# Kernel optimization log

Hardware: AMD Instinct MI355X
Metric: run time of the kernel (lower is better)

Reference implementation:

```python
import jax, jax.numpy as jnp
import numpy as np

N = 177          # hardcoded in update(): view(1, 177, out_channels)
HEADS = 1
OUT = 128
EDGE_DIM = 1
NEG_SLOPE = 0.2
E = 500000


def _glorot(key, shape):
    stdv = np.sqrt(6.0 / (shape[-2] + shape[-1])).astype(np.float32)
    return jax.random.uniform(key, shape, jnp.float32, -stdv, stdv)


def setup_inputs() -> dict:
    key = jax.random.key(0)
    ks = jax.random.split(key, 6)
    x = jax.random.normal(ks[0], (1, N, 128), jnp.float32)
    edge_index = jax.random.randint(ks[1], (2, E), 0, N)
    edge_attr = jax.random.normal(ks[2], (E, EDGE_DIM), jnp.float32)
    weight = _glorot(ks[3], (128, HEADS * OUT))
    att = _glorot(ks[4], (1, HEADS, 2 * OUT + EDGE_DIM))
    edge_update1 = _glorot(ks[5], (OUT + EDGE_DIM, OUT))
    bias = jnp.zeros((OUT,), jnp.float32)
    return {"x": x, "edge_attr": edge_attr, "weight": weight, "att": att,
            "edge_update1": edge_update1, "bias": bias, "edge_index": edge_index}


def reference(x, edge_attr, weight, att, edge_update1, bias, edge_index):
    # node transform: [N, in] @ [in, H*C] -> [N, H, C]
    h = (x[0] @ weight).reshape(-1, HEADS, OUT)
    src, dst = edge_index[0], edge_index[1]   # PyG: row 0 = source (j), row 1 = target (i)
    x_j = h[src]                              # [E, H, C]
    x_i = h[dst]                              # [E, H, C]
    ea = jnp.broadcast_to(edge_attr[:, None, :], (edge_attr.shape[0], HEADS, EDGE_DIM))
    x_j = jnp.concatenate([x_j, ea], axis=-1)              # [E, H, C+edge_dim]
    # attention logits: sum over feature axis of cat([x_i, x_j]) * att
    alpha = (jnp.concatenate([x_i, x_j], axis=-1) * att).sum(axis=-1)  # [E, H]
    alpha = jax.nn.leaky_relu(alpha, NEG_SLOPE)
    # scatter softmax over target nodes (two-pass: segment max then segment sum)
    amax = jax.ops.segment_max(alpha, dst, num_segments=N)             # [N, H]
    e = jnp.exp(alpha - amax[dst])
    esum = jax.ops.segment_sum(e, dst, num_segments=N)                 # [N, H]
    alpha = e / (esum[dst] + 1e-16)
    # weighted messages, scatter-add aggregation
    msg = x_j * alpha[:, :, None]                                      # [E, H, C+edge_dim]
    aggr = jax.ops.segment_sum(msg, dst, num_segments=N)               # [N, H, C+edge_dim]
    out = aggr.mean(axis=1) @ edge_update1 + bias                      # [N, C]
    return out.reshape(1, N, OUT)
```

## Files before the change

### kernel.cpp

```cpp
#include <hip/hip_runtime.h>

#define NN 177
#define NEG 0.2f
#define QR 45
#define ROWP 180
#define QSLOTS_P (QR * ROWP)
#define SL 8192
#define NCHUNK 64
#define EBLOCKS (NCHUNK * 4)
#define ETH 512

#define AIP_OFF  0
#define AJP_OFF  384
#define PART_OFF 768

__device__ __forceinline__ float4 f4add(float4 a, float4 b) {
    return make_float4(a.x + b.x, a.y + b.y, a.z + b.z, a.w + b.w);
}

__global__ __launch_bounds__(256)
void k_nodeA(const float* __restrict__ x, const float* __restrict__ w,
             const float* __restrict__ att, float* __restrict__ ws) {
    const int n = blockIdx.x, half = blockIdx.y;
    const int tid = threadIdx.x;
    const int j = tid & 63, kq = tid >> 6;
    __shared__ float xl[128];
    __shared__ float ph[256];
    if (tid < 128) xl[tid] = x[n * 128 + tid];
    __syncthreads();
    const float* wp = w + (size_t)(kq * 32) * 128 + half * 64 + j;
    float acc = 0.f;
#pragma unroll 8
    for (int k = 0; k < 32; ++k) acc += xl[kq * 32 + k] * wp[(size_t)k * 128];
    ph[tid] = acc;
    __syncthreads();
    if (tid < 64) {
        float hv = ph[j] + ph[64 + j] + ph[128 + j] + ph[192 + j];
        float pa = hv * att[half * 64 + j];
        float pb = hv * att[128 + half * 64 + j];
#pragma unroll
        for (int m = 1; m < 64; m <<= 1) {
            pa += __shfl_xor(pa, m);
            pb += __shfl_xor(pb, m);
        }
        if (j == 0) {
            ws[AIP_OFF + 2 * n + half] = pa;
            ws[AJP_OFF + 2 * n + half] = pb;
        }
    }
}

__global__ __launch_bounds__(ETH, 8)
void k_edge(const int* __restrict__ ei, const float* __restrict__ ea,
            const float* __restrict__ att, float* __restrict__ ws, int E, int CH) {
    const int chunk = blockIdx.x & (NCHUNK - 1), q = blockIdx.x >> 6;
    const int dlo = q * QR;
    int drows = NN - dlo; if (drows > QR) drows = QR;
    __shared__ __align__(16) float Wl[QSLOTS_P];
    __shared__ float ajl[NN], ailq[QR], Mq[QR], llast[QR], mred[64];
    int tid = threadIdx.x;
    const float4 z4 = make_float4(0.f, 0.f, 0.f, 0.f);
    for (int i = tid; i < QSLOTS_P / 4; i += ETH) ((float4*)Wl)[i] = z4;
    for (int i = tid; i < NN; i += ETH)
        ajl[i] = ws[AJP_OFF + 2 * i] + ws[AJP_OFF + 2 * i + 1];
    if (tid < QR) llast[tid] = 0.f;
    __syncthreads();
    if (tid < 64) {
        float m = -1e30f;
        for (int i = tid; i < NN; i += 64) m = fmaxf(m, ajl[i]);
        mred[tid] = m;
    }
    __syncthreads();
    if (tid < 16) mred[tid] = fmaxf(fmaxf(mred[tid], mred[tid + 16]),
                                    fmaxf(mred[tid + 32], mred[tid + 48]));
    __syncthreads();
    if (tid < 4) mred[tid] = fmaxf(fmaxf(mred[tid], mred[tid + 4]),
                                   fmaxf(mred[tid + 8], mred[tid + 12]));
    __syncthreads();
    if (tid == 0) mred[0] = fmaxf(fmaxf(mred[0], mred[1]), fmaxf(mred[2], mred[3]));
    __syncthreads();
    const float ajmax = mred[0];
    if (tid < drows) {
        float a = ws[AIP_OFF + 2 * (dlo + tid)] + ws[AIP_OFF + 2 * (dlo + tid) + 1];
        ailq[tid] = a;
        float M = a + ajmax + 1.0f;
        Mq[tid] = (M > 0.f) ? M : NEG * M;
    }
    const float cc = att[2 * 128];
    __syncthreads();

    const int base = chunk * CH;
    int lim = base + CH; if (lim > E) lim = E;
    const bool aligned4 = ((E & 3) == 0);
    for (int e0 = base + tid * 4; e0 < lim; e0 += ETH * 4) {
        int4 sv, dv; float4 eav;
        if (aligned4 && e0 + 3 < lim) {
            sv  = *(const int4*)(ei + e0);
            dv  = *(const int4*)(ei + E + e0);
            eav = *(const float4*)(ea + e0);
        } else {
            int e1 = lim - e0;
            sv.x = (e1 > 0) ? ei[e0]     : 0; dv.x = (e1 > 0) ? ei[E + e0]     : -1; eav.x = (e1 > 0) ? ea[e0]     : 0.f;
            sv.y = (e1 > 1) ? ei[e0 + 1] : 0; dv.y = (e1 > 1) ? ei[E + e0 + 1] : -1; eav.y = (e1 > 1) ? ea[e0 + 1] : 0.f;
            sv.z = (e1 > 2) ? ei[e0 + 2] : 0; dv.z = (e1 > 2) ? ei[E + e0 + 2] : -1; eav.z = (e1 > 2) ? ea[e0 + 2] : 0.f;
            sv.w = (e1 > 3) ? ei[e0 + 3] : 0; dv.w = (e1 > 3) ? ei[E + e0 + 3] : -1; eav.w = (e1 > 3) ? ea[e0 + 3] : 0.f;
        }
#define PROC(SS, DD, EE) do {                                   \
            int d_ = (DD) - dlo;                                \
            if ((unsigned)d_ < (unsigned)drows) {               \
                float t_ = ailq[d_] + ajl[SS] + cc * (EE);      \
                t_ = (t_ > 0.f) ? t_ : NEG * t_;                \
                float ev_ = __expf(t_ - Mq[d_]);                \
                atomicAdd(&Wl[d_ * ROWP + (SS)], ev_);          \
                atomicAdd(&llast[d_], ev_ * (EE));              \
            }                                                   \
        } while (0)
        PROC(sv.x, dv.x, eav.x);
        PROC(sv.y, dv.y, eav.y);
        PROC(sv.z, dv.z, eav.z);
        PROC(sv.w, dv.w, eav.w);
#undef PROC
    }
    __syncthreads();
    float* part = ws + PART_OFF + (size_t)blockIdx.x * SL;
    for (int i = tid; i < QSLOTS_P / 4; i += ETH)
        ((float4*)part)[i] = ((const float4*)Wl)[i];
    if (tid < QR) part[QSLOTS_P + tid] = llast[tid];
}

__global__ __launch_bounds__(ETH)
void k_outD(const float* __restrict__ ws, const float* __restrict__ x,
            const float* __restrict__ w, const float* __restrict__ eu,
            const float* __restrict__ bias, float* __restrict__ out) {
    __shared__ __align__(16) float wl[ROWP];
    __shared__ float red[128];
    __shared__ float sc[2];
    __shared__ float yl[128], vl[128];
    __shared__ __align__(16) float pd[2048];
    const int n = blockIdx.x, tid = threadIdx.x;
    const int q = n / QR, r = n % QR;
    const size_t qbase = PART_OFF + (size_t)q * NCHUNK * SL;

    {
        const int lane = tid & 63, cg = tid >> 6;
        const int s4 = lane * 4;
        float4 acc = make_float4(0.f, 0.f, 0.f, 0.f);
        if (s4 < ROWP) {
            const float* p = ws + qbase + (size_t)(cg * 8) * SL + (size_t)r * ROWP + s4;
#pragma unroll
            for (int ch = 0; ch < 8; ++ch)
                acc = f4add(acc, *(const float4*)(p + (size_t)ch * SL));
        }
        ((float4*)pd)[tid] = acc;
    }
    if (tid < 64) red[tid] = ws[qbase + (size_t)tid * SL + QSLOTS_P + r];
    __syncthreads();
    if (tid < 256) ((float4*)pd)[tid] = f4add(((float4*)pd)[tid], ((float4*)pd)[tid + 256]);
    if (tid < 32) red[tid] += red[tid + 32];
    __syncthreads();
    if (tid < 128) ((float4*)pd)[tid] = f4add(((float4*)pd)[tid], ((float4*)pd)[tid + 128]);
    if (tid < 16) red[tid] += red[tid + 16];
    __syncthreads();
    if (tid < 64) {
        float4 v = f4add(((float4*)pd)[tid], ((float4*)pd)[tid + 64]);
        if (tid * 4 < ROWP) ((float4*)wl)[tid] = v;
    }
    if (tid < 8) red[tid] += red[tid + 8];
    __syncthreads();
    if (tid == 0) {
        float wv = 0.f;
#pragma unroll
        for (int i = 0; i < 8; ++i) wv += red[i];
        sc[0] = wv;
    }
    __syncthreads();
    if (tid < 128) red[tid] = wl[tid] + ((tid + 128 < NN) ? wl[tid + 128] : 0.f);
    __syncthreads();
    for (int off = 64; off > 0; off >>= 1) {
        if (tid < off) red[tid] += red[tid + off];
        __syncthreads();
    }
    if (tid == 0) sc[1] = red[0];
    __syncthreads();

    const int c = tid & 127, g = tid >> 7;

    {
        float acc = 0.f;
        int s0 = g * 45, s1 = s0 + 45; if (s1 > NN) s1 = NN;
        for (int s = s0; s < s1; ++s) acc += wl[s] * x[s * 128 + c];
        pd[tid] = acc;
    }
    __syncthreads();
    if (tid < 128) yl[tid] = (pd[tid] + pd[128 + tid]) + (pd[256 + tid] + pd[384 + tid]);
    __syncthreads();

    {
        float acc = 0.f;
        const float* wp = w + (size_t)(g * 32) * 128 + c;
#pragma unroll 8
        for (int k = 0; k < 32; ++k) acc += yl[g * 32 + k] * wp[(size_t)k * 128];
        pd[tid] = acc;
    }
    __syncthreads();
    if (tid < 128) vl[tid] = (pd[tid] + pd[128 + tid]) + (pd[256 + tid] + pd[384 + tid]);
    __syncthreads();

    {
        float acc = 0.f;
        const float* ep = eu + (size_t)(g * 32) * 128 + c;
#pragma unroll 8
        for (int k = 0; k < 32; ++k) acc += vl[g * 32 + k] * ep[(size_t)k * 128];
        pd[tid] = acc;
    }
    __syncthreads();
    if (tid < 128) {
        float dot = (pd[tid] + pd[128 + tid]) + (pd[256 + tid] + pd[384 + tid]);
        out[n * 128 + tid] = (dot + sc[0] * eu[128 * 128 + tid]) / (sc[1] + 1e-16f) + bias[tid];
    }
}

extern "C" void kernel_launch(void* const* d_in, const int* in_sizes, int n_in,
                              void* d_out, int out_size, void* d_ws, size_t ws_size,
                              hipStream_t stream) {
    const float* x     = (const float*)d_in[0];
    const float* eattr = (const float*)d_in[1];
    const float* w     = (const float*)d_in[2];
    const float* att   = (const float*)d_in[3];
    const float* eu    = (const float*)d_in[4];
    const float* bias  = (const float*)d_in[5];
    const int*   ei    = (const int*)d_in[6];
    int E = in_sizes[6] / 2;
    int CH = (((E + NCHUNK - 1) / NCHUNK) + 3) & ~3;
    float* ws = (float*)d_ws;

    k_nodeA<<<dim3(NN, 2), 256, 0, stream>>>(x, w, att, ws);
    k_edge<<<EBLOCKS, ETH, 0, stream>>>(ei, eattr, att, ws, E, CH);
    k_outD<<<NN, ETH, 0, stream>>>(ws, x, w, eu, bias, (float*)d_out);
}
```

Before: 32.24 us.

## Fuse node attention projection into edge kernel via precomputed W·att vectors

Measured after the change: 34.71 us. 1.08x slower.

```diff
diff --git a/kernel.cpp b/kernel.cpp
--- a/kernel.cpp
+++ b/kernel.cpp
@@ -9,62 +9,76 @@
 #define NCHUNK 64
 #define EBLOCKS (NCHUNK * 4)
 #define ETH 512
-
-#define AIP_OFF  0
-#define AJP_OFF  384
+#define XFLOATS (NN * 128)
+
 #define PART_OFF 768
 
 __device__ __forceinline__ float4 f4add(float4 a, float4 b) {
     return make_float4(a.x + b.x, a.y + b.y, a.z + b.z, a.w + b.w);
 }
 
-__global__ __launch_bounds__(256)
-void k_nodeA(const float* __restrict__ x, const float* __restrict__ w,
-             const float* __restrict__ att, float* __restrict__ ws) {
-    const int n = blockIdx.x, half = blockIdx.y;
+__global__ __launch_bounds__(ETH)
+void k_edgeA(const float* __restrict__ x, const float* __restrict__ ea,
+             const float* __restrict__ w, const float* __restrict__ att,
+             const int* __restrict__ ei, float* __restrict__ ws, int E, int CH) {
+    extern __shared__ __align__(16) float big[];
+    __shared__ float atl[257], uvec[128], vvec[128];
+    __shared__ float pa_arr[2 * NN], pb_arr[2 * NN];
+    __shared__ float ail[NN], ajl[NN], Mq[QR], llast[QR], mred[64];
     const int tid = threadIdx.x;
-    const int j = tid & 63, kq = tid >> 6;
-    __shared__ float xl[128];
-    __shared__ float ph[256];
-    if (tid < 128) xl[tid] = x[n * 128 + tid];
-    __syncthreads();
-    const float* wp = w + (size_t)(kq * 32) * 128 + half * 64 + j;
-    float acc = 0.f;
-#pragma unroll 8
-    for (int k = 0; k < 32; ++k) acc += xl[kq * 32 + k] * wp[(size_t)k * 128];
-    ph[tid] = acc;
-    __syncthreads();
-    if (tid < 64) {
-        float hv = ph[j] + ph[64 + j] + ph[128 + j] + ph[192 + j];
-        float pa = hv * att[half * 64 + j];
-        float pb = hv * att[128 + half * 64 + j];
-#pragma unroll
-        for (int m = 1; m < 64; m <<= 1) {
-            pa += __shfl_xor(pa, m);
-            pb += __shfl_xor(pb, m);
-        }
-        if (j == 0) {
-            ws[AIP_OFF + 2 * n + half] = pa;
-            ws[AJP_OFF + 2 * n + half] = pb;
-        }
-    }
-}
-
-__global__ __launch_bounds__(ETH, 8)
-void k_edge(const int* __restrict__ ei, const float* __restrict__ ea,
-            const float* __restrict__ att, float* __restrict__ ws, int E, int CH) {
-    const int chunk = blockIdx.x & (NCHUNK - 1), q = blockIdx.x >> 6;
+    const int bid = blockIdx.x;
+    const int chunk = bid & (NCHUNK - 1), q = bid >> 6;
     const int dlo = q * QR;
     int drows = NN - dlo; if (drows > QR) drows = QR;
-    __shared__ __align__(16) float Wl[QSLOTS_P];
-    __shared__ float ajl[NN], ailq[QR], Mq[QR], llast[QR], mred[64];
-    int tid = threadIdx.x;
-    const float4 z4 = make_float4(0.f, 0.f, 0.f, 0.f);
-    for (int i = tid; i < QSLOTS_P / 4; i += ETH) ((float4*)Wl)[i] = z4;
-    for (int i = tid; i < NN; i += ETH)
-        ajl[i] = ws[AJP_OFF + 2 * i] + ws[AJP_OFF + 2 * i + 1];
-    if (tid < QR) llast[tid] = 0.f;
-    __syncthreads();
+
+    for (int i = tid; i < 257; i += ETH) atl[i] = att[i];
+    __syncthreads();
+
+    const float4* w4 = (const float4*)w;
+#pragma unroll
+    for (int i = 0; i < 8; ++i) {
+        int f = i * 512 + tid;
+        int k = f >> 5, c4 = (f & 31) << 2;
+        float4 wv = w4[f];
+        float pu = wv.x*atl[c4]     + wv.y*atl[c4+1]     + wv.z*atl[c4+2]     + wv.w*atl[c4+3];
+        float pv = wv.x*atl[128+c4] + wv.y*atl[128+c4+1] + wv.z*atl[128+c4+2] + wv.w*atl[128+c4+3];
+#pragma unroll
+        for (int m = 1; m <= 16; m <<= 1) { pu += __shfl_xor(pu, m); pv += __shfl_xor(pv, m); }
+        if ((tid & 31) == 0) { uvec[k] = pu; vvec[k] = pv; }
+    }
+
+    {
+        const float4* x4 = (const float4*)x;
+        float4* b4 = (float4*)big;
+        for (int i = tid; i < XFLOATS / 4; i += ETH) b4[i] = x4[i];
+    }
+    __syncthreads();
+
+    {
+        const int r = (tid < NN) ? tid : tid - NN;
+        const int h = (tid < NN) ? 0 : 1;
+        if (tid < 2 * NN) {
+            const float* xr = big + r * 128 + h * 64;
+            const float* ur = uvec + h * 64;
+            const float* vr = vvec + h * 64;
+            float pa = 0.f, pb = 0.f;
+#pragma unroll 8
+            for (int kk = 0; kk < 64; ++kk) {
+                int k = (kk + r) & 63;
+                float xv = xr[k];
+                pa += xv * ur[k];
+                pb += xv * vr[k];
+            }
+            pa_arr[tid] = pa; pb_arr[tid] = pb;
+        }
+    }
+    __syncthreads();
+    if (tid < NN) {
+        ail[tid] = pa_arr[tid] + pa_arr[NN + tid];
+        ajl[tid] = pb_arr[tid] + pb_arr[NN + tid];
+    }
+    __syncthreads();
+
     if (tid < 64) {
         float m = -1e30f;
         for (int i = tid; i < NN; i += 64) m = fmaxf(m, ajl[i]);
@@ -80,13 +94,16 @@
     if (tid == 0) mred[0] = fmaxf(fmaxf(mred[0], mred[1]), fmaxf(mred[2], mred[3]));
     __syncthreads();
     const float ajmax = mred[0];
+
+    float* Wl = big;
+    const float4 z4 = make_float4(0.f, 0.f, 0.f, 0.f);
+    for (int i = tid; i < QSLOTS_P / 4; i += ETH) ((float4*)Wl)[i] = z4;
+    if (tid < QR) llast[tid] = 0.f;
     if (tid < drows) {
-        float a = ws[AIP_OFF + 2 * (dlo + tid)] + ws[AIP_OFF + 2 * (dlo + tid) + 1];
-        ailq[tid] = a;
-        float M = a + ajmax + 1.0f;
+        float M = ail[dlo + tid] + ajmax + 1.0f;
         Mq[tid] = (M > 0.f) ? M : NEG * M;
     }
-    const float cc = att[2 * 128];
+    const float cc = atl[256];
     __syncthreads();
 
     const int base = chunk * CH;
@@ -108,7 +125,7 @@
 #define PROC(SS, DD, EE) do {                                   \
             int d_ = (DD) - dlo;                                \
             if ((unsigned)d_ < (unsigned)drows) {               \
-                float t_ = ailq[d_] + ajl[SS] + cc * (EE);      \
+                float t_ = ail[dlo + d_] + ajl[SS] + cc * (EE); \
                 t_ = (t_ > 0.f) ? t_ : NEG * t_;                \
                 float ev_ = __expf(t_ - Mq[d_]);                \
                 atomicAdd(&Wl[d_ * ROWP + (SS)], ev_);          \
@@ -122,7 +139,7 @@
 #undef PROC
     }
     __syncthreads();
-    float* part = ws + PART_OFF + (size_t)blockIdx.x * SL;
+    float* part = ws + PART_OFF + (size_t)bid * SL;
     for (int i = tid; i < QSLOTS_P / 4; i += ETH)
         ((float4*)part)[i] = ((const float4*)Wl)[i];
     if (tid < QR) part[QSLOTS_P + tid] = llast[tid];
@@ -234,7 +251,8 @@
     int CH = (((E + NCHUNK - 1) / NCHUNK) + 3) & ~3;
     float* ws = (float*)d_ws;
 
-    k_nodeA<<<dim3(NN, 2), 256, 0, stream>>>(x, w, att, ws);
-    k_edge<<<EBLOCKS, ETH, 0, stream>>>(ei, eattr, att, ws, E, CH);
+    hipFuncSetAttribute((const void*)k_edgeA,
+                        hipFuncAttributeMaxDynamicSharedMemorySize, XFLOATS * 4);
+    k_edgeA<<<EBLOCKS, ETH, XFLOATS * 4, stream>>>(x, eattr, w, att, ei, ws, E, CH);
     k_outD<<<NN, ETH, 0, stream>>>(ws, x, w, eu, bias, (float*)d_out);
 }
```
